# Kernel tuning notes

Measured on AMD Instinct MI355X. Metric: run time of the kernel, lower is better.

The kernel has to match this reference:

```python
import jax, jax.numpy as jnp
import numpy as np

N = 50000
IN_CH = 128
OUT_CH = 64
H1, C1 = 8, 8


def gat_layer(x, src, dst, W, att_src, att_dst, bias, heads, out_ch, concat, n_nodes):
    # x: [N, F_in]; W: [F_in, heads*out_ch]; att_*: [heads, out_ch]; bias: [heads*out_ch] or [out_ch]
    h = (x @ W).reshape(n_nodes, heads, out_ch)              # [N,H,C]
    a_src = jnp.einsum('nhc,hc->nh', h, att_src)             # [N,H]
    a_dst = jnp.einsum('nhc,hc->nh', h, att_dst)             # [N,H]
    e = jax.nn.leaky_relu(a_src[src] + a_dst[dst], 0.2)      # [E,H]
    # segment softmax over incoming edges of each dst node
    m = jax.ops.segment_max(e, dst, num_segments=n_nodes)    # [N,H]
    p = jnp.exp(e - m[dst])                                  # [E,H]
    s = jax.ops.segment_sum(p, dst, num_segments=n_nodes)    # [N,H]
    alpha = p / (s[dst] + 1e-16)                             # [E,H]
    out = jax.ops.segment_sum(h[src] * alpha[:, :, None], dst, num_segments=n_nodes)  # [N,H,C]
    out = out.reshape(n_nodes, heads * out_ch) if concat else out.mean(axis=1)
    return out + bias


def setup_inputs() -> dict:
    key = jax.random.key(0)
    ks = jax.random.split(key, 12)
    E = 1600000
    x = jax.random.normal(ks[0], (N, IN_CH), dtype=jnp.float32)
    edge_index = jax.random.randint(ks[1], (2, E), 0, N, dtype=jnp.int64)
    sc = 0.1
    return {
        'x': x,
        'edge_index': edge_index,
        'W1': jax.random.normal(ks[2], (IN_CH, H1 * C1), dtype=jnp.float32) * sc,
        'att_src1': jax.random.normal(ks[3], (H1, C1), dtype=jnp.float32) * sc,
        'att_dst1': jax.random.normal(ks[4], (H1, C1), dtype=jnp.float32) * sc,
        'b1': jnp.zeros((H1 * C1,), dtype=jnp.float32),
        'W2': jax.random.normal(ks[5], (H1 * C1, OUT_CH), dtype=jnp.float32) * sc,
        'att_src2': jax.random.normal(ks[6], (1, OUT_CH), dtype=jnp.float32) * sc,
        'att_dst2': jax.random.normal(ks[7], (1, OUT_CH), dtype=jnp.float32) * sc,
        'b2': jnp.zeros((OUT_CH,), dtype=jnp.float32),
        'lin_W': jax.random.normal(ks[8], (OUT_CH, 1), dtype=jnp.float32) * sc,
        'lin_b': jnp.zeros((1,), dtype=jnp.float32),
    }


def reference(x, edge_index, W1, att_src1, att_dst1, b1, W2, att_src2, att_dst2, b2, lin_W, lin_b):
    # add self loops (PyG GATConv default)
    loops = jnp.arange(N, dtype=edge_index.dtype)
    src = jnp.concatenate([edge_index[0], loops])
    dst = jnp.concatenate([edge_index[1], loops])
    # dropout layers are identity in eval mode
    h = gat_layer(x, src, dst, W1, att_src1, att_dst1, b1, H1, C1, True, N)
    h = jax.nn.elu(h)
    h = gat_layer(h, src, dst, W2, att_src2, att_dst2, b2, 1, OUT_CH, False, N)
    return h @ lin_W + lin_b
```

## Files before the change

### kernel.cpp

```cpp
#include <hip/hip_runtime.h>
#include <hip/hip_bf16.h>
#include <math.h>

#define NN     50000
#define FIN    128
#define F1     64
#define NH1    8
#define F2     64

#define BSH    256
#define NB     ((NN + BSH - 1) / BSH)
#define BCAP   9472
#define PREB   13
#define MG1B   ((NN + 255) / 256)

typedef __bf16 bf16x8 __attribute__((ext_vector_type(8)));
typedef float  f32x4  __attribute__((ext_vector_type(4)));


__device__ __forceinline__ float loadF(const void* p, long long i, int fp32) {
    if (fp32) return ((const float*)p)[i];
    return __bfloat162float(((const __hip_bfloat16*)p)[i]);
}
__device__ __forceinline__ int loadI_nt(const void* p, long long i, int i64) {
    if (i64) return (int)__builtin_nontemporal_load(&((const long long*)p)[i]);
    return __builtin_nontemporal_load(&((const int*)p)[i]);
}
__device__ __forceinline__ unsigned short f2bfu(float f) {
    unsigned u = __float_as_uint(f);
    return (unsigned short)((u + 0x7FFFu + ((u >> 16) & 1u)) >> 16);
}
__device__ __forceinline__ float b2f(unsigned short u) {
    return __uint_as_float(((unsigned)u) << 16);
}


__global__ __launch_bounds__(1024) void k_front(
    const void* __restrict__ x, const void* __restrict__ ei, int E, int Etot,
    int* __restrict__ flags,
    const void* __restrict__ W1, const void* __restrict__ W2,
    unsigned short* __restrict__ W1p, unsigned short* __restrict__ W2p,
    int* __restrict__ bcnt, unsigned* __restrict__ binned) {
    __shared__ int s_a, s_b;
    __shared__ int hist[NB], gbase[NB];
    int tid = threadIdx.x;
    if (blockIdx.x < PREB) {
        if (tid == 0) { s_a = 0; s_b = 0; }
        __syncthreads();
        const unsigned short* u = (const unsigned short*)x;
        int cnt = 0;
        for (int i = tid; i < 8192; i += 1024) {
            unsigned short v = u[i];
            if ((v & 0x7F80) == 0x7F80) cnt++;
        }
        if (cnt) atomicAdd(&s_a, cnt);
        const unsigned* e32 = (const unsigned*)ei;
        int nz = 0;
        for (int i = tid; i < 2048; i += 1024) {
            if (e32[2 * i + 1] != 0u) nz++;
        }
        if (nz) atomicAdd(&s_b, nz);
        __syncthreads();
        int fp32 = (s_a > 2) ? 1 : 0;
        if (tid == 0 && blockIdx.x == 0) {
            flags[0] = fp32;
            flags[1] = (s_b == 0) ? 1 : 0;
        }
        int gt = blockIdx.x * 1024 + tid, gs = PREB * 1024;
        for (int i = gt; i < (FIN / 32) * 4 * 512; i += gs) {
            int j = i & 7, l = (i >> 3) & 63, f = i >> 9;
            int kb = f >> 2, nt = f & 3;
            int k = kb * 32 + (l >> 4) * 8 + j, n = nt * 16 + (l & 15);
            W1p[i] = f2bfu(loadF(W1, k * 64 + n, fp32));
        }
        for (int i = gt; i < (F1 / 32) * 4 * 512; i += gs) {
            int j = i & 7, l = (i >> 3) & 63, f = i >> 9;
            int kb = f >> 2, nt = f & 3;
            int k = kb * 32 + (l >> 4) * 8 + j, n = nt * 16 + (l & 15);
            W2p[i] = f2bfu(loadF(W2, k * 64 + n, fp32));
        }
    } else {
        if (tid == 0) s_b = 0;
        for (int i = tid; i < NB; i += 1024) hist[i] = 0;
        __syncthreads();
        const unsigned* e32 = (const unsigned*)ei;
        int nz = 0;
        for (int i = tid; i < 2048; i += 1024) {
            if (e32[2 * i + 1] != 0u) nz++;
        }
        if (nz) atomicAdd(&s_b, nz);
        __syncthreads();
        int i64 = (s_b == 0) ? 1 : 0;
        long long base = (long long)(blockIdx.x - PREB) * 8192;
        unsigned pk[8]; short bb[8];
        #pragma unroll
        for (int u = 0; u < 8; ++u) {
            long long j = base + u * 1024 + tid;
            int s = -1, d = -1;
            if (j < Etot) {
                if (j < E) { s = loadI_nt(ei, j, i64); d = loadI_nt(ei, (long long)E + j, i64); }
                else       { s = d = (int)(j - E); }
            }
            if ((unsigned)s < NN && (unsigned)d < NN) {
                bb[u] = (short)(d >> 8);
                pk[u] = ((unsigned)s << 8) | (unsigned)(d & 255);
                atomicAdd(&hist[bb[u]], 1);
            } else bb[u] = -1;
        }
        __syncthreads();
        for (int i = tid; i < NB; i += 1024) {
            int h = hist[i];
            gbase[i] = h ? atomicAdd(&bcnt[i], h) : 0;
            hist[i] = 0;
        }
        __syncthreads();
        #pragma unroll
        for (int u = 0; u < 8; ++u) {
            if (bb[u] >= 0) {
                int pos = gbase[bb[u]] + atomicAdd(&hist[bb[u]], 1);
                if (pos < BCAP) binned[(size_t)bb[u] * BCAP + pos] = pk[u];
            }
        }
    }
}


__global__ __launch_bounds__(1024) void k_mid(
    const int* __restrict__ bcnt, const unsigned* __restrict__ binned,
    int* __restrict__ offs, int* __restrict__ perm,
    const void* __restrict__ x, const unsigned short* __restrict__ W1p,
    const void* __restrict__ attS, const void* __restrict__ attD,
    __hip_bfloat16* __restrict__ h1, float* __restrict__ a1s,
    float* __restrict__ a1d, const int* __restrict__ flags) {
    __shared__ __align__(16) char smem[33280];
    int tid = threadIdx.x;
    if (blockIdx.x < NB) {
        int* hist = (int*)smem;
        int* cur  = (int*)(smem + 1024);
        int* sd   = (int*)(smem + 2048);
        int bk = blockIdx.x;
        int n0 = bk * BSH;
        if (tid < 256) sd[tid] = (tid < NB) ? min(bcnt[tid], BCAP) : 0;
        __syncthreads();
        for (int off = 1; off < BSH; off <<= 1) {
            int t = 0;
            if (tid < 256 && tid >= off) t = sd[tid - off];
            __syncthreads();
            if (tid < 256) sd[tid] += t;
            __syncthreads();
        }
        int gb = (bk > 0) ? sd[bk - 1] : 0;
        if (bk == 0 && tid == 0) offs[NN] = sd[NB - 1];
        __syncthreads();
        int cnt = bcnt[bk]; if (cnt > BCAP) cnt = BCAP;
        const unsigned* bp = binned + (size_t)bk * BCAP;
        if (tid < 256) hist[tid] = 0;
        __syncthreads();
        for (int i = tid; i < cnt; i += 1024)
            atomicAdd(&hist[bp[i] & 255], 1);
        __syncthreads();
        int myh = (tid < 256) ? hist[tid] : 0;
        if (tid < 256) sd[tid] = myh;
        __syncthreads();
        for (int off = 1; off < BSH; off <<= 1) {
            int t = 0;
            if (tid < 256 && tid >= off) t = sd[tid - off];
            __syncthreads();
            if (tid < 256) sd[tid] += t;
            __syncthreads();
        }
        if (tid < 256) {
            int excl = sd[tid] - myh;
            cur[tid] = gb + excl;
            if (n0 + tid < NN) offs[n0 + tid] = gb + excl;
        }
        __syncthreads();
        for (int i = tid; i < cnt; i += 1024) {
            unsigned pk = bp[i];
            int pos = atomicAdd(&cur[pk & 255], 1);
            perm[pos] = (int)(pk >> 8);
        }
    } else {
        int fp32 = flags[0];
        unsigned short* hl = (unsigned short*)smem;
        float* attSl = (float*)(smem + 32768);
        float* attDl = (float*)(smem + 32768 + 256);
        if (tid < 64) { attSl[tid] = loadF(attS, tid, fp32); attDl[tid] = loadF(attD, tid, fp32); }
        int sub = tid >> 8, t = tid & 255;
        int w = t >> 6, l = t & 63;
        int quad = l >> 4, lm = l & 15;
        int n0 = (blockIdx.x - NB) * 256 + sub * 64;
        unsigned short* hls = hl + sub * 4096;

        bf16x8 bfr[16];
        #pragma unroll
        for (int f = 0; f < 16; ++f)
            bfr[f] = *(const bf16x8*)(W1p + f * 512 + l * 8);

        int nodeA = n0 + w * 16 + lm;
        long long rowA = (nodeA < NN) ? nodeA : 0;
        f32x4 acc[4];
        #pragma unroll
        for (int nt = 0; nt < 4; ++nt) acc[nt] = (f32x4){0.f, 0.f, 0.f, 0.f};

        #pragma unroll
        for (int kb = 0; kb < 4; ++kb) {
            bf16x8 af;
            if (!fp32) {
                af = *(const bf16x8*)((const unsigned short*)x + rowA * FIN + kb * 32 + quad * 8);
            } else {
                const float* xf = (const float*)x + rowA * FIN + kb * 32 + quad * 8;
                union { unsigned short s[8]; bf16x8 v; } tmp;
                #pragma unroll
                for (int j = 0; j < 8; ++j) tmp.s[j] = f2bfu(xf[j]);
                af = tmp.v;
            }
            #pragma unroll
            for (int nt = 0; nt < 4; ++nt)
                acc[nt] = __builtin_amdgcn_mfma_f32_16x16x32_bf16(af, bfr[kb * 4 + nt], acc[nt], 0, 0, 0);
        }

        #pragma unroll
        for (int nt = 0; nt < 4; ++nt) {
            #pragma unroll
            for (int r = 0; r < 4; ++r) {
                int nl = w * 16 + quad * 4 + r;
                int node = n0 + nl;
                int c = nt * 16 + lm;
                unsigned short hb = f2bfu(acc[nt][r]);
                hls[nl * 64 + c] = hb;
                if (node < NN) ((unsigned short*)h1)[(size_t)node * 64 + c] = hb;
            }
        }
        __syncthreads();
        #pragma unroll
        for (int pp = 0; pp < 2; ++pp) {
            int p = t + pp * 256;
            int nl = p >> 3, g = p & 7;
            int node = n0 + nl;
            float ss = 0.f, dd = 0.f;
            #pragma unroll
            for (int j = 0; j < 8; ++j) {
                float hv = b2f(hls[nl * 64 + g * 8 + j]);
                ss += hv * attSl[g * 8 + j];
                dd += hv * attDl[g * 8 + j];
            }
            if (node < NN) {
                a1s[(size_t)node * NH1 + g] = ss;
                a1d[(size_t)node * NH1 + g] = dd;
            }
        }
    }
}


#define HLP 72

__global__ __launch_bounds__(256) void k_agg1f(
    const int* __restrict__ offs, const int* __restrict__ perm,
    const __hip_bfloat16* __restrict__ h1, const float* __restrict__ a1s,
    const float* __restrict__ a1d, const void* __restrict__ b1,
    const unsigned short* __restrict__ W2p,
    const void* __restrict__ attS2, const void* __restrict__ attD2,
    const void* __restrict__ linW,
    float2* __restrict__ g2s, float* __restrict__ a2d,
    int n, const int* __restrict__ flags) {
    int fp32 = flags[0];
    __shared__ unsigned short hl[16 * HLP];
    __shared__ float attSl[64], attDl[64];
    __shared__ float sp[16 * 4], dp[16 * 4], gp[16 * 4];
    int tid = threadIdx.x;
    if (tid < 64) { attSl[tid] = loadF(attS2, tid, fp32); attDl[tid] = loadF(attD2, tid, fp32); }
    int w = tid >> 6, c = tid & 63;
    int n0 = blockIdx.x * 16;
    int u = c & 7, h = c >> 3, cb = c & 56;
    const unsigned short* hu = (const unsigned short*)h1;

    for (int m = 0; m < 4; ++m) {
        int d = n0 + w * 4 + m;
        if (d < n) {
            int start = offs[d], end = offs[d + 1];
            float adl = a1d[(size_t)d * NH1 + h];
            float acc = 0.f, denp = 0.f;
            for (int i = start; i < end; i += 8) {
                int j = i + u;
                int jc = (j < end) ? j : (end - 1);
                int sj = perm[jc];
                float e = a1s[(size_t)sj * NH1 + h] + adl;
                e = fmaxf(e, 0.2f * e);
                float p = (j < end) ? __expf(e) : 0.f;
                denp += p;
                #pragma unroll
                for (int k = 0; k < 8; ++k) {
                    int su = __builtin_amdgcn_readlane(sj, k);
                    float pk = __shfl(p, cb + k, 64);
                    acc = fmaf(pk, b2f(hu[(size_t)su * 64 + c]), acc);
                }
            }
            denp += __shfl_xor(denp, 1, 64);
            denp += __shfl_xor(denp, 2, 64);
            denp += __shfl_xor(denp, 4, 64);
            float v = acc / (denp + 1e-16f) + loadF(b1, c, fp32);
            v = (v > 0.f) ? v : expm1f(v);
            hl[(w * 4 + m) * HLP + c] = f2bfu(v);
        }
    }
    __syncthreads();

    int quad = c >> 4, lm = c & 15;
    bf16x8 bf0 = *(const bf16x8*)(W2p + (0 * 4 + w) * 512 + c * 8);
    bf16x8 bf1 = *(const bf16x8*)(W2p + (1 * 4 + w) * 512 + c * 8);
    bf16x8 af0 = *(const bf16x8*)(hl + lm * HLP + 0 * 32 + quad * 8);
    bf16x8 af1 = *(const bf16x8*)(hl + lm * HLP + 1 * 32 + quad * 8);
    f32x4 acc2 = (f32x4){0.f, 0.f, 0.f, 0.f};
    acc2 = __builtin_amdgcn_mfma_f32_16x16x32_bf16(af0, bf0, acc2, 0, 0, 0);
    acc2 = __builtin_amdgcn_mfma_f32_16x16x32_bf16(af1, bf1, acc2, 0, 0, 0);

    int cg = w * 16 + lm;
    float aSc = attSl[cg], aDc = attDl[cg];
    float lWc = loadF(linW, cg, fp32);
    #pragma unroll
    for (int r = 0; r < 4; ++r) {
        int nl = quad * 4 + r;
        unsigned short hb = f2bfu(acc2[r]);
        float hv = b2f(hb);
        float pvs = hv * aSc, pvd = hv * aDc, pvg = hv * lWc;
        pvs += __shfl_xor(pvs, 1, 64); pvd += __shfl_xor(pvd, 1, 64); pvg += __shfl_xor(pvg, 1, 64);
        pvs += __shfl_xor(pvs, 2, 64); pvd += __shfl_xor(pvd, 2, 64); pvg += __shfl_xor(pvg, 2, 64);
        pvs += __shfl_xor(pvs, 4, 64); pvd += __shfl_xor(pvd, 4, 64); pvg += __shfl_xor(pvg, 4, 64);
        pvs += __shfl_xor(pvs, 8, 64); pvd += __shfl_xor(pvd, 8, 64); pvg += __shfl_xor(pvg, 8, 64);
        if (lm == 0) { sp[nl * 4 + w] = pvs; dp[nl * 4 + w] = pvd; gp[nl * 4 + w] = pvg; }
    }
    __syncthreads();
    if (tid < 16) {
        int node = n0 + tid;
        if (node < n) {
            float ss = sp[tid * 4 + 0] + sp[tid * 4 + 1] + sp[tid * 4 + 2] + sp[tid * 4 + 3];
            float dd = dp[tid * 4 + 0] + dp[tid * 4 + 1] + dp[tid * 4 + 2] + dp[tid * 4 + 3];
            float gg = gp[tid * 4 + 0] + gp[tid * 4 + 1] + gp[tid * 4 + 2] + gp[tid * 4 + 3];
            g2s[node] = make_float2(ss, gg);
            a2d[node] = dd;
        }
    }
}


__global__ __launch_bounds__(256) void k_agg2(
    const int* __restrict__ offs, const int* __restrict__ perm,
    const float2* __restrict__ g2s, const float* __restrict__ a2d,
    const void* __restrict__ b2, const void* __restrict__ linW,
    const void* __restrict__ linb,
    void* __restrict__ out, int n, const int* __restrict__ flags) {
    int fp32 = flags[0];
    int w = threadIdx.x >> 6, c = threadIdx.x & 63;
    int d = blockIdx.x * 4 + w;
    if (d >= n) return;
    int start = offs[d], end = offs[d + 1];
    float ad = a2d[d];
    float acc = 0.f, den = 0.f;
    for (int i = start + c; i < end; i += 64) {
        int s = perm[i];
        float2 ag = g2s[s];
        float e = ag.x + ad;
        e = fmaxf(e, 0.2f * e);
        float p = __expf(e);
        acc = fmaf(p, ag.y, acc);
        den += p;
    }
    float cst = loadF(b2, c, fp32) * loadF(linW, c, fp32);
    #pragma unroll
    for (int off = 1; off < 64; off <<= 1) {
        acc += __shfl_xor(acc, off, 64);
        den += __shfl_xor(den, off, 64);
        cst += __shfl_xor(cst, off, 64);
    }
    if (c == 0) {
        float r = acc / (den + 1e-16f) + cst + loadF(linb, 0, fp32);
        if (fp32) ((float*)out)[d] = r;
        else      ((__hip_bfloat16*)out)[d] = __float2bfloat16(r);
    }
}


static inline char* carve(char*& p, size_t bytes) {
    char* r = p;
    p += (bytes + 255) & ~size_t(255);
    return r;
}

extern "C" void kernel_launch(void* const* d_in, const int* in_sizes, int n_in,
                              void* d_out, int out_size, void* d_ws, size_t ws_size,
                              hipStream_t stream) {
    const void* x     = d_in[0];
    const void* ei    = d_in[1];
    const void* W1    = d_in[2];
    const void* attS1 = d_in[3];
    const void* attD1 = d_in[4];
    const void* b1    = d_in[5];
    const void* W2    = d_in[6];
    const void* attS2 = d_in[7];
    const void* attD2 = d_in[8];
    const void* b2    = d_in[9];
    const void* linW  = d_in[10];
    const void* linb  = d_in[11];

    int E    = in_sizes[1] / 2;
    int Etot = E + NN;

    char* p = (char*)d_ws;
    int*   flags = (int*)carve(p, 256);
    int*   bcnt  = (int*)carve(p, (size_t)NB * 4);
    unsigned short* W1p = (unsigned short*)carve(p, 8192 * 2);
    unsigned short* W2p = (unsigned short*)carve(p, 4096 * 2);
    int*   offs  = (int*)carve(p, (size_t)(NN + 1) * 4);
    int*   perm  = (int*)carve(p, (size_t)Etot * 4);
    unsigned* binned = (unsigned*)carve(p, (size_t)NB * BCAP * 4);
    float*    a1s    = (float*)carve(p, (size_t)NN * NH1 * 4);
    float*    a1d    = (float*)carve(p, (size_t)NN * NH1 * 4);
    __hip_bfloat16* h1 = (__hip_bfloat16*)carve(p, (size_t)NN * F1 * 2);
    float2* g2s = (float2*)carve(p, (size_t)NN * 8);
    float*  a2d = (float*)carve(p, (size_t)NN * 4);

    hipMemsetAsync(bcnt, 0, (size_t)NB * 4, stream);

    int nbin = (Etot + 8191) / 8192;
    k_front<<<PREB + nbin, 1024, 0, stream>>>(x, ei, E, Etot, flags,
                                              W1, W2, W1p, W2p, bcnt, binned);
    k_mid<<<NB + MG1B, 1024, 0, stream>>>(bcnt, binned, offs, perm,
                                          x, W1p, attS1, attD1, h1, a1s, a1d, flags);
    k_agg1f<<<(NN + 15) / 16, 256, 0, stream>>>(offs, perm, h1, a1s, a1d, b1,
                                                W2p, attS2, attD2, linW, g2s, a2d, NN, flags);
    k_agg2<<<(NN + 3) / 4, 256, 0, stream>>>(offs, perm, g2s, a2d, b2, linW, linb, d_out, NN, flags);
}
```

Before: 203.0 us.

## Use per-bucket fixed CSR offsets and one wave per node in layer-1 aggregation

The global prefix scan over bucket counts in k_mid is dropped. Each bucket now writes its edges at a fixed base (bucket*BCAP), with separate start and end arrays per destination, so k_mid does less block-wide synchronisation and the perm buffer grows to NB*BCAP. k_agg1f now launches 1024 threads per block so each of 16 waves handles one destination node instead of 4 waves looping over 4 nodes each, which exposes more parallelism for the latency-bound gathers. The MFMA epilogue is restricted to the first 256 threads, leaving 12 waves idle after the barrier.

```diff
diff --git a/kernel.cpp b/kernel.cpp
--- a/kernel.cpp
+++ b/kernel.cpp
@@ -127,7 +127,7 @@
 
 __global__ __launch_bounds__(1024) void k_mid(
     const int* __restrict__ bcnt, const unsigned* __restrict__ binned,
-    int* __restrict__ offs, int* __restrict__ perm,
+    int* __restrict__ dstart, int* __restrict__ dend, int* __restrict__ perm,
     const void* __restrict__ x, const unsigned short* __restrict__ W1p,
     const void* __restrict__ attS, const void* __restrict__ attD,
     __hip_bfloat16* __restrict__ h1, float* __restrict__ a1s,
@@ -140,7 +140,16 @@
         int* sd   = (int*)(smem + 2048);
         int bk = blockIdx.x;
         int n0 = bk * BSH;
-        if (tid < 256) sd[tid] = (tid < NB) ? min(bcnt[tid], BCAP) : 0;
+        int gb = bk * BCAP;
+        int cnt = bcnt[bk]; if (cnt > BCAP) cnt = BCAP;
+        const unsigned* bp = binned + (size_t)bk * BCAP;
+        if (tid < 256) hist[tid] = 0;
+        __syncthreads();
+        for (int i = tid; i < cnt; i += 1024)
+            atomicAdd(&hist[bp[i] & 255], 1);
+        __syncthreads();
+        int myh = (tid < 256) ? hist[tid] : 0;
+        if (tid < 256) sd[tid] = myh;
         __syncthreads();
         for (int off = 1; off < BSH; off <<= 1) {
             int t = 0;
@@ -149,30 +158,13 @@
             if (tid < 256) sd[tid] += t;
             __syncthreads();
         }
-        int gb = (bk > 0) ? sd[bk - 1] : 0;
-        if (bk == 0 && tid == 0) offs[NN] = sd[NB - 1];
-        __syncthreads();
-        int cnt = bcnt[bk]; if (cnt > BCAP) cnt = BCAP;
-        const unsigned* bp = binned + (size_t)bk * BCAP;
-        if (tid < 256) hist[tid] = 0;
-        __syncthreads();
-        for (int i = tid; i < cnt; i += 1024)
-            atomicAdd(&hist[bp[i] & 255], 1);
-        __syncthreads();
-        int myh = (tid < 256) ? hist[tid] : 0;
-        if (tid < 256) sd[tid] = myh;
-        __syncthreads();
-        for (int off = 1; off < BSH; off <<= 1) {
-            int t = 0;
-            if (tid < 256 && tid >= off) t = sd[tid - off];
-            __syncthreads();
-            if (tid < 256) sd[tid] += t;
-            __syncthreads();
-        }
         if (tid < 256) {
             int excl = sd[tid] - myh;
             cur[tid] = gb + excl;
-            if (n0 + tid < NN) offs[n0 + tid] = gb + excl;
+            if (n0 + tid < NN) {
+                dstart[n0 + tid] = gb + excl;
+                dend[n0 + tid]   = gb + excl + myh;
+            }
         }
         __syncthreads();
         for (int i = tid; i < cnt; i += 1024) {
@@ -256,8 +248,9 @@
 
 #define HLP 72
 
-__global__ __launch_bounds__(256) void k_agg1f(
-    const int* __restrict__ offs, const int* __restrict__ perm,
+__global__ __launch_bounds__(1024) void k_agg1f(
+    const int* __restrict__ dstart, const int* __restrict__ dend,
+    const int* __restrict__ perm,
     const __hip_bfloat16* __restrict__ h1, const float* __restrict__ a1s,
     const float* __restrict__ a1d, const void* __restrict__ b1,
     const unsigned short* __restrict__ W2p,
@@ -271,65 +264,66 @@
     __shared__ float sp[16 * 4], dp[16 * 4], gp[16 * 4];
     int tid = threadIdx.x;
     if (tid < 64) { attSl[tid] = loadF(attS2, tid, fp32); attDl[tid] = loadF(attD2, tid, fp32); }
-    int w = tid >> 6, c = tid & 63;
+    int wave = tid >> 6, c = tid & 63;
     int n0 = blockIdx.x * 16;
     int u = c & 7, h = c >> 3, cb = c & 56;
     const unsigned short* hu = (const unsigned short*)h1;
 
-    for (int m = 0; m < 4; ++m) {
-        int d = n0 + w * 4 + m;
-        if (d < n) {
-            int start = offs[d], end = offs[d + 1];
-            float adl = a1d[(size_t)d * NH1 + h];
-            float acc = 0.f, denp = 0.f;
-            for (int i = start; i < end; i += 8) {
-                int j = i + u;
-                int jc = (j < end) ? j : (end - 1);
-                int sj = perm[jc];
-                float e = a1s[(size_t)sj * NH1 + h] + adl;
-                e = fmaxf(e, 0.2f * e);
-                float p = (j < end) ? __expf(e) : 0.f;
-                denp += p;
-                #pragma unroll
-                for (int k = 0; k < 8; ++k) {
-                    int su = __builtin_amdgcn_readlane(sj, k);
-                    float pk = __shfl(p, cb + k, 64);
-                    acc = fmaf(pk, b2f(hu[(size_t)su * 64 + c]), acc);
-                }
-            }
-            denp += __shfl_xor(denp, 1, 64);
-            denp += __shfl_xor(denp, 2, 64);
-            denp += __shfl_xor(denp, 4, 64);
-            float v = acc / (denp + 1e-16f) + loadF(b1, c, fp32);
-            v = (v > 0.f) ? v : expm1f(v);
-            hl[(w * 4 + m) * HLP + c] = f2bfu(v);
-        }
+    int d = n0 + wave;
+    if (d < n) {
+        int start = dstart[d], end = dend[d];
+        float adl = a1d[(size_t)d * NH1 + h];
+        float acc = 0.f, denp = 0.f;
+        for (int i = start; i < end; i += 8) {
+            int j = i + u;
+            int jc = (j < end) ? j : (end - 1);
+            int sj = perm[jc];
+            float e = a1s[(size_t)sj * NH1 + h] + adl;
+            e = fmaxf(e, 0.2f * e);
+            float p = (j < end) ? __expf(e) : 0.f;
+            denp += p;
+            #pragma unroll
+            for (int k = 0; k < 8; ++k) {
+                int su = __builtin_amdgcn_readlane(sj, k);
+                float pk = __shfl(p, cb + k, 64);
+                acc = fmaf(pk, b2f(hu[(size_t)su * 64 + c]), acc);
+            }
+        }
+        denp += __shfl_xor(denp, 1, 64);
+        denp += __shfl_xor(denp, 2, 64);
+        denp += __shfl_xor(denp, 4, 64);
+        float v = acc / (denp + 1e-16f) + loadF(b1, c, fp32);
+        v = (v > 0.f) ? v : expm1f(v);
+        hl[wave * HLP + c] = f2bfu(v);
     }
     __syncthreads();
 
-    int quad = c >> 4, lm = c & 15;
-    bf16x8 bf0 = *(const bf16x8*)(W2p + (0 * 4 + w) * 512 + c * 8);
-    bf16x8 bf1 = *(const bf16x8*)(W2p + (1 * 4 + w) * 512 + c * 8);
-    bf16x8 af0 = *(const bf16x8*)(hl + lm * HLP + 0 * 32 + quad * 8);
-    bf16x8 af1 = *(const bf16x8*)(hl + lm * HLP + 1 * 32 + quad * 8);
-    f32x4 acc2 = (f32x4){0.f, 0.f, 0.f, 0.f};
-    acc2 = __builtin_amdgcn_mfma_f32_16x16x32_bf16(af0, bf0, acc2, 0, 0, 0);
-    acc2 = __builtin_amdgcn_mfma_f32_16x16x32_bf16(af1, bf1, acc2, 0, 0, 0);
-
-    int cg = w * 16 + lm;
-    float aSc = attSl[cg], aDc = attDl[cg];
-    float lWc = loadF(linW, cg, fp32);
-    #pragma unroll
-    for (int r = 0; r < 4; ++r) {
-        int nl = quad * 4 + r;
-        unsigned short hb = f2bfu(acc2[r]);
-        float hv = b2f(hb);
-        float pvs = hv * aSc, pvd = hv * aDc, pvg = hv * lWc;
-        pvs += __shfl_xor(pvs, 1, 64); pvd += __shfl_xor(pvd, 1, 64); pvg += __shfl_xor(pvg, 1, 64);
-        pvs += __shfl_xor(pvs, 2, 64); pvd += __shfl_xor(pvd, 2, 64); pvg += __shfl_xor(pvg, 2, 64);
-        pvs += __shfl_xor(pvs, 4, 64); pvd += __shfl_xor(pvd, 4, 64); pvg += __shfl_xor(pvg, 4, 64);
-        pvs += __shfl_xor(pvs, 8, 64); pvd += __shfl_xor(pvd, 8, 64); pvg += __shfl_xor(pvg, 8, 64);
-        if (lm == 0) { sp[nl * 4 + w] = pvs; dp[nl * 4 + w] = pvd; gp[nl * 4 + w] = pvg; }
+    if (tid < 256) {
+        int w = tid >> 6;
+        int quad = c >> 4, lm = c & 15;
+        bf16x8 bf0 = *(const bf16x8*)(W2p + (0 * 4 + w) * 512 + c * 8);
+        bf16x8 bf1 = *(const bf16x8*)(W2p + (1 * 4 + w) * 512 + c * 8);
+        bf16x8 af0 = *(const bf16x8*)(hl + lm * HLP + 0 * 32 + quad * 8);
+        bf16x8 af1 = *(const bf16x8*)(hl + lm * HLP + 1 * 32 + quad * 8);
+        f32x4 acc2 = (f32x4){0.f, 0.f, 0.f, 0.f};
+        acc2 = __builtin_amdgcn_mfma_f32_16x16x32_bf16(af0, bf0, acc2, 0, 0, 0);
+        acc2 = __builtin_amdgcn_mfma_f32_16x16x32_bf16(af1, bf1, acc2, 0, 0, 0);
+
+        int cg = w * 16 + lm;
+        float aSc = attSl[cg], aDc = attDl[cg];
+        float lWc = loadF(linW, cg, fp32);
+        #pragma unroll
+        for (int r = 0; r < 4; ++r) {
+            int nl = quad * 4 + r;
+            unsigned short hb = f2bfu(acc2[r]);
+            float hv = b2f(hb);
+            float pvs = hv * aSc, pvd = hv * aDc, pvg = hv * lWc;
+            pvs += __shfl_xor(pvs, 1, 64); pvd += __shfl_xor(pvd, 1, 64); pvg += __shfl_xor(pvg, 1, 64);
+            pvs += __shfl_xor(pvs, 2, 64); pvd += __shfl_xor(pvd, 2, 64); pvg += __shfl_xor(pvg, 2, 64);
+            pvs += __shfl_xor(pvs, 4, 64); pvd += __shfl_xor(pvd, 4, 64); pvg += __shfl_xor(pvg, 4, 64);
+            pvs += __shfl_xor(pvs, 8, 64); pvd += __shfl_xor(pvd, 8, 64); pvg += __shfl_xor(pvg, 8, 64);
+            if (lm == 0) { sp[nl * 4 + w] = pvs; dp[nl * 4 + w] = pvd; gp[nl * 4 + w] = pvg; }
+        }
     }
     __syncthreads();
     if (tid < 16) {
@@ -346,7 +340,8 @@
 
 
 __global__ __launch_bounds__(256) void k_agg2(
-    const int* __restrict__ offs, const int* __restrict__ perm,
+    const int* __restrict__ dstart, const int* __restrict__ dend,
+    const int* __restrict__ perm,
     const float2* __restrict__ g2s, const float* __restrict__ a2d,
     const void* __restrict__ b2, const void* __restrict__ linW,
     const void* __restrict__ linb,
@@ -355,7 +350,7 @@
     int w = threadIdx.x >> 6, c = threadIdx.x & 63;
     int d = blockIdx.x * 4 + w;
     if (d >= n) return;
-    int start = offs[d], end = offs[d + 1];
+    int start = dstart[d], end = dend[d];
     float ad = a2d[d];
     float acc = 0.f, den = 0.f;
     for (int i = start + c; i < end; i += 64) {
@@ -412,8 +407,9 @@
     int*   bcnt  = (int*)carve(p, (size_t)NB * 4);
     unsigned short* W1p = (unsigned short*)carve(p, 8192 * 2);
     unsigned short* W2p = (unsigned short*)carve(p, 4096 * 2);
-    int*   offs  = (int*)carve(p, (size_t)(NN + 1) * 4);
-    int*   perm  = (int*)carve(p, (size_t)Etot * 4);
+    int*   dstart = (int*)carve(p, (size_t)NN * 4);
+    int*   dend   = (int*)carve(p, (size_t)NN * 4);
+    int*   perm   = (int*)carve(p, (size_t)NB * BCAP * 4);
     unsigned* binned = (unsigned*)carve(p, (size_t)NB * BCAP * 4);
     float*    a1s    = (float*)carve(p, (size_t)NN * NH1 * 4);
     float*    a1d    = (float*)carve(p, (size_t)NN * NH1 * 4);
@@ -426,9 +422,9 @@
     int nbin = (Etot + 8191) / 8192;
     k_front<<<PREB + nbin, 1024, 0, stream>>>(x, ei, E, Etot, flags,
                                               W1, W2, W1p, W2p, bcnt, binned);
-    k_mid<<<NB + MG1B, 1024, 0, stream>>>(bcnt, binned, offs, perm,
+    k_mid<<<NB + MG1B, 1024, 0, stream>>>(bcnt, binned, dstart, dend, perm,
                                           x, W1p, attS1, attD1, h1, a1s, a1d, flags);
-    k_agg1f<<<(NN + 15) / 16, 256, 0, stream>>>(offs, perm, h1, a1s, a1d, b1,
-                                                W2p, attS2, attD2, linW, g2s, a2d, NN, flags);
-    k_agg2<<<(NN + 3) / 4, 256, 0, stream>>>(offs, perm, g2s, a2d, b2, linW, linb, d_out, NN, flags);
-}
+    k_agg1f<<<(NN + 15) / 16, 1024, 0, stream>>>(dstart, dend, perm, h1, a1s, a1d, b1,
+                                                 W2p, attS2, attD2, linW, g2s, a2d, NN, flags);
+    k_agg2<<<(NN + 3) / 4, 256, 0, stream>>>(dstart, dend, perm, g2s, a2d, b2, linW, linb, d_out, NN, flags);
+}
```

New measurement: 206.6 us. No clear change (+1.8%).
